# Optimization experiments

Measured on AMD Instinct MI355X. Metric: run time of the kernel, lower is better.

Reference implementation:

```python
import jax, jax.numpy as jnp
import numpy as np

C_CURV = 1.0      # curvature
EPS = 1e-4        # matches torch epsilon=0.0001
ATTN_SCALE = 0.12
NUM_HEADS = 16
HEAD_DIM = 64


def _sqnorm(x):
    return jnp.sum(x * x, axis=-1, keepdims=True)


def mobius_add(x, y, c):
    xn2, yn2 = _sqnorm(x), _sqnorm(y)
    ip = jnp.sum(x * y, axis=-1, keepdims=True)
    num = (1 + 2 * c * ip + c * yn2) * x + (1 - c * xn2) * y
    den = jnp.maximum(1 + 2 * c * ip + c * c * xn2 * yn2, EPS)
    return num / den


def logmap(x, u, c):
    sf = 2.0 / (1.0 + c * _sqnorm(x))                      # scaling factor at x
    mob = mobius_add(-x, u, c)
    mn = jnp.sqrt(_sqnorm(mob))
    cf = 2.0 / (sf * jnp.sqrt(c) + EPS)
    arg = jnp.clip(jnp.sqrt(c * mn), -0.99, 0.99)          # matches torch clamp on sqrt(c*norm)
    return cf * jnp.arctanh(arg) * mob / (mn + EPS)


def expmap(x, v, c):
    sf = 2.0 / (1.0 + c * _sqnorm(x))
    vn = jnp.sqrt(_sqnorm(v))
    arg = jnp.sqrt(jnp.clip(c * sf * vn * vn / 2.0, 0.0, 8.0))
    second = (1.0 / jnp.sqrt(c)) * jnp.tanh(arg) * v / (vn + EPS)
    return mobius_add(x, second, c)


def rms_norm(x):
    return x * jax.lax.rsqrt(jnp.mean(x * x, axis=-1, keepdims=True) + 1.1920929e-07)


def rotary_tables(T, head_dim):
    # dim//4 geometric freqs, padded with dim//4 zeros -> dim//2 total
    freqs = (1.0 / 1024.0) ** jnp.linspace(0.0, 1.0, head_dim // 4, dtype=jnp.float32)
    freqs = jnp.concatenate([freqs, jnp.zeros(head_dim // 4, dtype=jnp.float32)])
    theta = jnp.arange(T, dtype=jnp.float32)[:, None] * freqs[None, :]   # [T, hd/2]
    return jnp.cos(theta), jnp.sin(theta)


def apply_rotary(x, cos, sin):
    # x: [B,T,H,hd]; cos/sin: [T,hd/2]
    x1, x2 = jnp.split(x, 2, axis=-1)
    c = cos[None, :, None, :]
    s = sin[None, :, None, :]
    return jnp.concatenate([x1 * c + x2 * s, -x1 * s + x2 * c], axis=-1)


def setup_inputs() -> dict:
    key = jax.random.key(0)
    k1, k2, k3 = jax.random.split(key, 3)
    B, T, dim = 1, 2048, 1024
    hdim = NUM_HEADS * HEAD_DIM
    std = 0.5 * dim ** (-0.5)
    bound = (3.0 ** 0.5) * std
    x = jax.random.normal(k1, (B, T, dim), dtype=jnp.float32)
    qkv_w = jax.random.uniform(k2, (3, hdim, dim), dtype=jnp.float32, minval=-bound, maxval=bound)
    # original zero-inits c_proj; use small random weights for a non-degenerate baseline
    c_proj_w = jax.random.uniform(k3, (dim, hdim), dtype=jnp.float32, minval=-bound, maxval=bound)
    return {"x": x, "qkv_w": qkv_w, "c_proj_w": c_proj_w}


def reference(x, qkv_w, c_proj_w):
    B, T, dim = x.shape
    H, hd = NUM_HEADS, HEAD_DIM
    c = C_CURV

    # reference point: previous token (origin for first position)
    ref = jnp.pad(x[:, :-1, :], ((0, 0), (1, 0), (0, 0)))
    x_hyp = logmap(ref, x, c)

    # fused QKV projection: [B,T,3*hdim] -> q,k,v [B,T,H,hd]
    qkv = jnp.einsum('btd,ehd->bteh', x_hyp, qkv_w)            # e=3, h=hdim
    q, k, v = (qkv[:, :, i, :].reshape(B, T, H, hd) for i in range(3))

    cos, sin = rotary_tables(T, hd)
    q = apply_rotary(rms_norm(q), cos, sin)
    k = apply_rotary(rms_norm(k), cos, sin)

    # causal attention with fixed scale 0.12 (BlockMask here = standard causal)
    scores = jnp.einsum('bqhd,bkhd->bhqk', q, k) * ATTN_SCALE
    causal = jnp.tril(jnp.ones((T, T), dtype=bool))
    scores = jnp.where(causal[None, None], scores, -jnp.inf)
    p = jax.nn.softmax(scores, axis=-1)
    y = jnp.einsum('bhqk,bkhd->bqhd', p, v).reshape(B, T, H * hd)

    y = y @ c_proj_w.T
    y = expmap(ref, y, c)   # map_back_after_attention=True
    return y, ref
```

## Files before the change

kernel.cpp:

```cpp
#include <hip/hip_runtime.h>
#include <math.h>

#define T_SEQ 2048
#define DIM   1024
#define HD3   3072
#define NH    16
#define HD    64
#define EPSF  1e-4f
#define MB    1048576

typedef __attribute__((ext_vector_type(8))) short bf16x8;
typedef __attribute__((ext_vector_type(4))) float f32x4;
typedef __attribute__((ext_vector_type(16))) float f32x16;
typedef __attribute__((ext_vector_type(4))) unsigned int u32x4;

__device__ __forceinline__ ushort f2bf(float f) {
  unsigned int u = __float_as_uint(f);
  unsigned int r = (u + 0x7FFFu + ((u >> 16) & 1u)) >> 16;
  return (ushort)r;
}
__device__ __forceinline__ float bf2f(ushort u) {
  return __uint_as_float(((unsigned int)u) << 16);
}
__device__ __forceinline__ unsigned int pk2(float a, float b) {
  unsigned int r;
  asm("v_cvt_pk_bf16_f32 %0, %1, %2" : "=v"(r) : "v"(a), "v"(b));
  return r;
}

#define GLOAD(gp, lp) __builtin_amdgcn_global_load_lds( \
    (const __attribute__((address_space(1))) unsigned int*)(gp), \
    (__attribute__((address_space(3))) unsigned int*)(lp), 16, 0, 0)

__device__ __forceinline__ float blockSum(float v, float* s4) {
#pragma unroll
  for (int o = 32; o > 0; o >>= 1) v += __shfl_xor(v, o, 64);
  __syncthreads();
  if ((threadIdx.x & 63) == 0) s4[threadIdx.x >> 6] = v;
  __syncthreads();
  return s4[0] + s4[1] + s4[2] + s4[3];
}

__global__ void logmap_cvt(const float* __restrict__ x,
                           ushort* __restrict__ xhyp,
                           float* __restrict__ ref_out,
                           const float* __restrict__ wa,
                           const float* __restrict__ wb,
                           ushort* __restrict__ da,
                           ushort* __restrict__ db) {
  if (blockIdx.x >= T_SEQ) {
    int i = (blockIdx.x - T_SEQ) * 256 + threadIdx.x;
    const float* src; ushort* dst; int j;
    if (i < 393216) { src = wa; dst = da; j = i; }
    else            { src = wb; dst = db; j = i - 393216; }
    float4 a = ((const float4*)src)[j * 2];
    float4 b = ((const float4*)src)[j * 2 + 1];
    bf16x8 v;
    v[0] = f2bf(a.x); v[1] = f2bf(a.y); v[2] = f2bf(a.z); v[3] = f2bf(a.w);
    v[4] = f2bf(b.x); v[5] = f2bf(b.y); v[6] = f2bf(b.z); v[7] = f2bf(b.w);
    *(bf16x8*)(dst + (size_t)j * 8) = v;
    return;
  }
  __shared__ float s4[4];
  int t = blockIdx.x;
  const float* xt = x + (size_t)t * DIM;
  float xe[4], re[4];
  float xn2 = 0.f, yn2 = 0.f, ip = 0.f;
#pragma unroll
  for (int i = 0; i < 4; i++) {
    int e = threadIdx.x + i * 256;
    float xv = xt[e];
    float rv = (t > 0) ? xt[e - DIM] : 0.f;
    xe[i] = xv; re[i] = rv;
    yn2 += xv * xv;
    xn2 += rv * rv;
    ip  -= rv * xv;
    ref_out[(size_t)t * DIM + e] = rv;
  }
  xn2 = blockSum(xn2, s4);
  yn2 = blockSum(yn2, s4);
  ip  = blockSum(ip,  s4);
  float a = 1.f + 2.f * ip + yn2;
  float b = 1.f - xn2;
  float den = fmaxf(1.f + 2.f * ip + xn2 * yn2, EPSF);
  float invden = 1.f / den;
  float mob[4];
  float mn2 = 0.f;
#pragma unroll
  for (int i = 0; i < 4; i++) {
    float m = (-a * re[i] + b * xe[i]) * invden;
    mob[i] = m;
    mn2 += m * m;
  }
  mn2 = blockSum(mn2, s4);
  float mn  = sqrtf(mn2);
  float sf  = 2.f / (1.f + xn2);
  float cf  = 2.f / (sf + EPSF);
  float arg = fminf(sqrtf(mn), 0.99f);
  float mult = cf * atanhf(arg) / (mn + EPSF);
#pragma unroll
  for (int i = 0; i < 4; i++)
    xhyp[(size_t)t * DIM + threadIdx.x + i * 256] = f2bf(mult * mob[i]);
}

template<int BM>
__global__ __launch_bounds__(256) void gemm_bf16(const ushort* __restrict__ A,
                                                 const ushort* __restrict__ W,
                                                 float* __restrict__ C,
                                                 int M, int N, int K) {
  __shared__ ushort As[2][BM * 32];
  __shared__ ushort Bs[2][128 * 32];
  constexpr int NF = (BM == 128) ? 4 : 2;
  int tid = threadIdx.x;
  int lane = tid & 63, w = tid >> 6;
  int row_base = (BM == 128) ? (w >> 1) * 64 : 0;
  int col_base = (BM == 128) ? (w & 1) * 64 : w * 32;
  int g = lane >> 4, cc = lane & 15;
  int bm = blockIdx.y * BM, bn = blockIdx.x * 128;
  f32x4 acc[4][NF] = {};

  {
    if constexpr (BM == 128) {
#pragma unroll
      for (int i = 0; i < 2; i++) {
        int ch = i * 256 + tid;
        GLOAD(A + (size_t)(bm + (ch >> 2)) * K + (ch & 3) * 8, &As[0][ch * 8]);
      }
    } else {
      int ch = tid;
      GLOAD(A + (size_t)(bm + (ch >> 2)) * K + (ch & 3) * 8, &As[0][ch * 8]);
    }
#pragma unroll
    for (int i = 0; i < 2; i++) {
      int ch = i * 256 + tid;
      GLOAD(W + (size_t)(bn + (ch >> 2)) * K + (ch & 3) * 8, &Bs[0][ch * 8]);
    }
  }
  __syncthreads();

  int cur = 0;
  for (int kt = 0; kt < K; kt += 32) {
    if (kt + 32 < K) {
      int nxt = cur ^ 1;
      if constexpr (BM == 128) {
#pragma unroll
        for (int i = 0; i < 2; i++) {
          int ch = i * 256 + tid;
          GLOAD(A + (size_t)(bm + (ch >> 2)) * K + kt + 32 + (ch & 3) * 8, &As[nxt][ch * 8]);
        }
      } else {
        int ch = tid;
        GLOAD(A + (size_t)(bm + (ch >> 2)) * K + kt + 32 + (ch & 3) * 8, &As[nxt][ch * 8]);
      }
#pragma unroll
      for (int i = 0; i < 2; i++) {
        int ch = i * 256 + tid;
        GLOAD(W + (size_t)(bn + (ch >> 2)) * K + kt + 32 + (ch & 3) * 8, &Bs[nxt][ch * 8]);
      }
    }
    bf16x8 af[4], bfr[NF];
#pragma unroll
    for (int m = 0; m < 4; m++)
      af[m] = *(const bf16x8*)&As[cur][(row_base + m * 16 + cc) * 32 + 8 * g];
#pragma unroll
    for (int n = 0; n < NF; n++)
      bfr[n] = *(const bf16x8*)&Bs[cur][(col_base + n * 16 + cc) * 32 + 8 * g];
#pragma unroll
    for (int m = 0; m < 4; m++)
#pragma unroll
      for (int n = 0; n < NF; n++)
        acc[m][n] = __builtin_amdgcn_mfma_f32_16x16x32_bf16(af[m], bfr[n], acc[m][n], 0, 0, 0);
    __syncthreads();
    cur ^= 1;
  }
#pragma unroll
  for (int m = 0; m < 4; m++)
#pragma unroll
    for (int n = 0; n < NF; n++)
#pragma unroll
      for (int j = 0; j < 4; j++)
        C[(size_t)(bm + row_base + m * 16 + g * 4 + j) * N + bn + col_base + n * 16 + cc] = acc[m][n][j];
}

__global__ __launch_bounds__(256) void rmsrot_vtrans(const float* __restrict__ qkvf,
                                                     ushort* __restrict__ qfr,
                                                     ushort* __restrict__ kfr,
                                                     ushort* __restrict__ vfr) {
  __shared__ ushort qtile[64][64];
  __shared__ ushort ktile[64][64];
  __shared__ ushort vtile[64][64];
  int h = blockIdx.y, tt = blockIdx.x;
  int w = threadIdx.x >> 6, lane = threadIdx.x & 63;
  int j = lane & 31;
  float freq = 0.f;
  bool dotrig = (j < 16);
  if (dotrig) freq = exp2f(-(10.f / 15.f) * (float)j);
#pragma unroll 4
  for (int i = 0; i < 16; i++) {
    int r = w * 16 + i;
    int t = tt * 64 + r;
    const float* base = qkvf + (size_t)t * HD3;
    float qv = base[h * HD + lane];
    float kv = base[DIM + h * HD + lane];
    float qs = qv * qv, ks = kv * kv;
#pragma unroll
    for (int o = 32; o > 0; o >>= 1) {
      qs += __shfl_xor(qs, o, 64);
      ks += __shfl_xor(ks, o, 64);
    }
    float qn = qv * rsqrtf(qs * (1.f / 64.f) + 1.1920929e-07f);
    float kn = kv * rsqrtf(ks * (1.f / 64.f) + 1.1920929e-07f);
    float cth = 1.f, sth = 0.f;
    if (dotrig) {
      float th = (float)t * freq;
      cth = cosf(th);
      sth = sinf(th);
    }
    float qp = __shfl_xor(qn, 32, 64);
    float kp = __shfl_xor(kn, 32, 64);
    float sgn = (lane < 32) ? 1.f : -1.f;
    int pc = lane ^ ((r & 7) << 3);
    qtile[r][pc] = f2bf(qn * cth + sgn * qp * sth);
    ktile[r][pc] = f2bf(kn * cth + sgn * kp * sth);
  }
#pragma unroll
  for (int i = 0; i < 16; i++) {
    int r = w + i * 4;
    vtile[lane][r ^ ((lane & 7) << 3)] =
        f2bf(qkvf[(size_t)(tt * 64 + r) * HD3 + 2 * DIM + h * HD + lane]);
  }
  __syncthreads();
#pragma unroll
  for (int rd = 0; rd < 6; rd++) {
    int item = rd * 256 + threadIdx.x;
    int buf = item >> 9;
    int grp = (item >> 8) & 1;
    int st  = (item >> 6) & 3;
    int ln  = item & 63;
    int row = grp * 32 + (ln & 31);
    int col = st * 16 + 8 * (ln >> 5);
    int pc  = col ^ ((row & 7) << 3);
    bf16x8 v8;
    if (buf == 0)      v8 = *(const bf16x8*)&qtile[row][pc];
    else if (buf == 1) v8 = *(const bf16x8*)&ktile[row][pc];
    else               v8 = *(const bf16x8*)&vtile[row][pc];
    if (buf == 0) {
      size_t dst = (((size_t)h * 64 + tt * 2 + grp) * 4 + st) * 512 + ln * 8;
      *(bf16x8*)&qfr[dst] = v8;
    } else {
      size_t dst = ((((size_t)h * 32 + tt) * 2 + grp) * 4 + st) * 512 + ln * 8;
      if (buf == 1) *(bf16x8*)&kfr[dst] = v8;
      else          *(bf16x8*)&vfr[dst] = v8;
    }
  }
}

__global__ __launch_bounds__(256, 2) void attn_mfma(const ushort* __restrict__ qfr,
                                                    const ushort* __restrict__ kfr,
                                                    const ushort* __restrict__ vfr,
                                                    ushort* __restrict__ parts) {
  int lane = threadIdx.x & 63;
  int hi = lane >> 5;
  int q31 = lane & 31;
  int w = threadIdx.x >> 6;
  int tid = blockIdx.x * 4 + w;
  int h = tid / 288;
  int s = tid % 288;
  int g = (int)((sqrtf((float)s + 1.0f) - 1.0f) * 0.5f);
  while (4 * (g + 1) * (g + 2) <= s) ++g;
  while (4 * g * (g + 1) > s) --g;
  int rem = s - 4 * g * (g + 1);
  int qi8 = rem / (g + 1);
  int ch  = rem - qi8 * (g + 1);
  int qt  = 8 * g + qi8;
  int qbase  = qt * 32;
  int kstart = ch * 256;
  int kend   = min(kstart + 256, qbase + 32);
  bool fin   = (kend == qbase + 32);
  int nt     = (kend - kstart + 63) >> 6;

  bf16x8 qf[4];
  {
    const ushort* qb8 = qfr + (((size_t)h * 64 + qt) * 4) * 512 + lane * 8;
#pragma unroll
    for (int st = 0; st < 4; st++)
      qf[st] = *(const bf16x8*)(qb8 + st * 512);
  }

  f32x16 acc0 = {}, acc1 = {};
  float lrow = 0.f;
  int qglob = qbase + q31;
  const float SC = 0.12f * 1.44269504f;

  for (int ti = 0; ti < nt; ti++) {
    int k0 = kstart + ti * 64;
    int kblk = k0 >> 6;
    const ushort* kb8 = kfr + ((((size_t)h * 32 + kblk) * 2) * 4) * 512 + lane * 8;
    const ushort* vb8 = vfr + ((((size_t)h * 32 + kblk) * 2) * 4) * 512 + lane * 8;
    f32x16 cA = {}, cB = {};
#pragma unroll
    for (int st = 0; st < 4; st++) {
      bf16x8 kfa = *(const bf16x8*)(kb8 + st * 512);
      bf16x8 kfb = *(const bf16x8*)(kb8 + (4 + st) * 512);
      cA = __builtin_amdgcn_mfma_f32_32x32x16_bf16(kfa, qf[st], cA, 0, 0, 0);
      cB = __builtin_amdgcn_mfma_f32_32x32x16_bf16(kfb, qf[st], cB, 0, 0, 0);
    }
    float p[32];
#pragma unroll
    for (int r = 0; r < 16; r++) {
      float sA = cA[r] * SC;
      float sB = cB[r] * SC;
      if (fin) {
        int key = k0 + (r & 3) + 8 * (r >> 2) + 4 * hi;
        if (key > qglob)      sA = -1e30f;
        if (key + 32 > qglob) sB = -1e30f;
      }
      p[r] = sA;
      p[16 + r] = sB;
    }
    float rs0 = 0.f, rs1 = 0.f;
#pragma unroll
    for (int r = 0; r < 16; r++) {
      p[r]      = exp2f(p[r]);      rs0 += p[r];
      p[16 + r] = exp2f(p[16 + r]); rs1 += p[16 + r];
    }
    float rs = rs0 + rs1;
    rs += __shfl_xor(rs, 32, 64);
    lrow += rs;
    unsigned int pw[16], sw[16];
#pragma unroll
    for (int j = 0; j < 16; j++)
      pw[j] = pk2(p[2 * j], p[2 * j + 1]);
#pragma unroll
    for (int j = 0; j < 16; j++)
      sw[j] = __shfl_xor(pw[j], 32, 64);
    u32x4 u0, u1, u2, u3;
    u0[0] = hi ? sw[2]  : pw[0];
    u0[1] = hi ? sw[3]  : pw[1];
    u0[2] = hi ? pw[2]  : sw[0];
    u0[3] = hi ? pw[3]  : sw[1];
    u1[0] = hi ? sw[6]  : pw[4];
    u1[1] = hi ? sw[7]  : pw[5];
    u1[2] = hi ? pw[6]  : sw[4];
    u1[3] = hi ? pw[7]  : sw[5];
    u2[0] = hi ? sw[10] : pw[8];
    u2[1] = hi ? sw[11] : pw[9];
    u2[2] = hi ? pw[10] : sw[8];
    u2[3] = hi ? pw[11] : sw[9];
    u3[0] = hi ? sw[14] : pw[12];
    u3[1] = hi ? sw[15] : pw[13];
    u3[2] = hi ? pw[14] : sw[12];
    u3[3] = hi ? pw[15] : sw[13];
    bf16x8 pbA0 = __builtin_bit_cast(bf16x8, u0);
    bf16x8 pbA1 = __builtin_bit_cast(bf16x8, u1);
    bf16x8 pbB0 = __builtin_bit_cast(bf16x8, u2);
    bf16x8 pbB1 = __builtin_bit_cast(bf16x8, u3);
    {
      bf16x8 vA0 = *(const bf16x8*)(vb8 + 0 * 512);
      bf16x8 vA1 = *(const bf16x8*)(vb8 + 1 * 512);
      bf16x8 vA2 = *(const bf16x8*)(vb8 + 2 * 512);
      bf16x8 vA3 = *(const bf16x8*)(vb8 + 3 * 512);
      acc0 = __builtin_amdgcn_mfma_f32_32x32x16_bf16(vA0, pbA0, acc0, 0, 0, 0);
      acc0 = __builtin_amdgcn_mfma_f32_32x32x16_bf16(vA1, pbA1, acc0, 0, 0, 0);
      acc0 = __builtin_amdgcn_mfma_f32_32x32x16_bf16(vA2, pbB0, acc0, 0, 0, 0);
      acc0 = __builtin_amdgcn_mfma_f32_32x32x16_bf16(vA3, pbB1, acc0, 0, 0, 0);
      bf16x8 vB0 = *(const bf16x8*)(vb8 + 4 * 512);
      bf16x8 vB1 = *(const bf16x8*)(vb8 + 5 * 512);
      bf16x8 vB2 = *(const bf16x8*)(vb8 + 6 * 512);
      bf16x8 vB3 = *(const bf16x8*)(vb8 + 7 * 512);
      acc1 = __builtin_amdgcn_mfma_f32_32x32x16_bf16(vB0, pbA0, acc1, 0, 0, 0);
      acc1 = __builtin_amdgcn_mfma_f32_32x32x16_bf16(vB1, pbA1, acc1, 0, 0, 0);
      acc1 = __builtin_amdgcn_mfma_f32_32x32x16_bf16(vB2, pbB0, acc1, 0, 0, 0);
      acc1 = __builtin_amdgcn_mfma_f32_32x32x16_bf16(vB3, pbB1, acc1, 0, 0, 0);
    }
  }
  ushort* rec = parts + (size_t)(h * 288 + s) * 2176;
#pragma unroll
  for (int r = 0; r < 16; r++) {
    int d = (r & 3) + 8 * (r >> 2) + 4 * hi;
    rec[q31 * 64 + d]      = f2bf(acc0[r]);
    rec[q31 * 64 + 32 + d] = f2bf(acc1[r]);
  }
  if (!hi)
    *(float*)((char*)rec + 4096 + q31 * 4) = lrow;
}

__global__ __launch_bounds__(256) void attn_merge(const ushort* __restrict__ parts,
                                                  ushort* __restrict__ o) {
  int w = threadIdx.x >> 6, lane = threadIdx.x & 63;
  int idx = blockIdx.x * 4 + w;
  int r = idx & 31;
  int rec_i = idx >> 5;
  int qt = rec_i & 63, h = rec_i >> 6;
  int g = qt >> 3, rr = qt & 7;
  int nch = g + 1;
  int off = qt + 4 * g * (g - 1) + rr * g;
  const ushort* base = parts + (size_t)(h * 288 + off) * 2176;
  float L = 0.f, ov = 0.f;
#pragma unroll
  for (int i = 0; i < 8; i++) {
    if (i < nch) {
      L  += *(const float*)((const char*)base + i * 4352 + 4096 + r * 4);
      ov += bf2f(base[i * 2176 + r * 64 + lane]);
    }
  }
  o[(size_t)(qt * 32 + r) * DIM + h * HD + lane] = f2bf(ov / L);
}

__global__ void expmap_kernel(const float* __restrict__ y2,
                              const float* __restrict__ ref,
                              float* __restrict__ yout) {
  __shared__ float s4[4];
  int t = blockIdx.x;
  float xe[4], ve[4];
  float xn2 = 0.f, vn2 = 0.f, xv = 0.f;
#pragma unroll
  for (int i = 0; i < 4; i++) {
    int e = threadIdx.x + i * 256;
    float X = ref[(size_t)t * DIM + e];
    float V = y2[(size_t)t * DIM + e];
    xe[i] = X; ve[i] = V;
    xn2 += X * X; vn2 += V * V; xv += X * V;
  }
  xn2 = blockSum(xn2, s4);
  vn2 = blockSum(vn2, s4);
  xv  = blockSum(xv,  s4);
  float vn  = sqrtf(vn2);
  float sf  = 2.f / (1.f + xn2);
  float arg = sqrtf(fminf(fmaxf(0.5f * sf * vn2, 0.f), 8.f));
  float scl = tanhf(arg) / (vn + EPSF);
  float yn2 = scl * scl * vn2;
  float ip  = scl * xv;
  float A = 1.f + 2.f * ip + yn2;
  float B = (1.f - xn2) * scl;
  float den = fmaxf(1.f + 2.f * ip + xn2 * yn2, EPSF);
  float invden = 1.f / den;
#pragma unroll
  for (int i = 0; i < 4; i++)
    yout[(size_t)t * DIM + threadIdx.x + i * 256] = (A * xe[i] + B * ve[i]) * invden;
}

extern "C" void kernel_launch(void* const* d_in, const int* in_sizes, int n_in,
                              void* d_out, int out_size, void* d_ws, size_t ws_size,
                              hipStream_t stream) {
  const float* x        = (const float*)d_in[0];
  const float* qkv_w    = (const float*)d_in[1];
  const float* c_proj_w = (const float*)d_in[2];
  float* out = (float*)d_out;
  char*  W   = (char*)d_ws;

  ushort* qkvw_bf   = (ushort*)(W);
  ushort* cprojw_bf = (ushort*)(W + 6  * MB);
  ushort* xhyp_bf   = (ushort*)(W + 8  * MB);
  float*  qkvf      = (float*) (W + 12 * MB);
  ushort* qfrag     = (ushort*)(W + 36 * MB);
  ushort* kfrag     = (ushort*)(W + 40 * MB);
  ushort* vfrag     = (ushort*)(W + 44 * MB);
  ushort* parts     = (ushort*)(W + 12 * MB);
  ushort* obuf      = xhyp_bf;
  float*  y2        = qkvf;
  float*  ref       = out + (size_t)T_SEQ * DIM;

  logmap_cvt<<<T_SEQ + 2048, 256, 0, stream>>>(x, xhyp_bf, ref, qkv_w, c_proj_w,
                                               qkvw_bf, cprojw_bf);
  gemm_bf16<128><<<dim3(HD3 / 128, T_SEQ / 128), 256, 0, stream>>>(xhyp_bf, qkvw_bf, qkvf, T_SEQ, HD3, DIM);
  rmsrot_vtrans<<<dim3(T_SEQ / 64, NH), 256, 0, stream>>>(qkvf, qfrag, kfrag, vfrag);
  attn_mfma<<<1152, 256, 0, stream>>>(qfrag, kfrag, vfrag, parts);
  attn_merge<<<8192, 256, 0, stream>>>(parts, obuf);
  gemm_bf16<64><<<dim3(DIM / 128, T_SEQ / 64), 256, 0, stream>>>(obuf, cprojw_bf, y2, T_SEQ, DIM, DIM);
  expmap_kernel<<<T_SEQ, 256, 0, stream>>>(y2, ref, out);
}
```

Before: 121.0 us.

## Fuse RMS norm, rotary and fragment layout into QKV GEMM epilogue

Removes the separate rmsrot_vtrans kernel by doing RMS normalisation, rotary embedding, bf16 conversion and the swizzled fragment layout (including the V transpose) directly in the QKV GEMM epilogue. Each wave's 64x64 accumulator tile maps to one head, so the row norm is reduced with lane shuffles. This avoids writing and re-reading the 24 MB fp32 QKV intermediate and saves one launch. In exchange it adds 32 KB of shared memory per block, which may lower GEMM occupancy, and puts more epilogue work on the GEMM.

Measured after the change: 109.1 us. 1.11x faster.

```diff
diff --git a/kernel.cpp b/kernel.cpp
--- a/kernel.cpp
+++ b/kernel.cpp
@@ -103,13 +103,17 @@
     xhyp[(size_t)t * DIM + threadIdx.x + i * 256] = f2bf(mult * mob[i]);
 }
 
-template<int BM>
+template<int BM, int EPI>
 __global__ __launch_bounds__(256) void gemm_bf16(const ushort* __restrict__ A,
                                                  const ushort* __restrict__ W,
                                                  float* __restrict__ C,
+                                                 ushort* __restrict__ qfr,
+                                                 ushort* __restrict__ kfr,
+                                                 ushort* __restrict__ vfr,
                                                  int M, int N, int K) {
   __shared__ ushort As[2][BM * 32];
   __shared__ ushort Bs[2][128 * 32];
+  __shared__ ushort etile[EPI ? 4 * 64 * 64 : 4];
   constexpr int NF = (BM == 128) ? 4 : 2;
   int tid = threadIdx.x;
   int lane = tid & 63, w = tid >> 6;
@@ -173,85 +177,81 @@
     __syncthreads();
     cur ^= 1;
   }
-#pragma unroll
-  for (int m = 0; m < 4; m++)
-#pragma unroll
-    for (int n = 0; n < NF; n++)
-#pragma unroll
-      for (int j = 0; j < 4; j++)
-        C[(size_t)(bm + row_base + m * 16 + g * 4 + j) * N + bn + col_base + n * 16 + cc] = acc[m][n][j];
-}
-
-__global__ __launch_bounds__(256) void rmsrot_vtrans(const float* __restrict__ qkvf,
-                                                     ushort* __restrict__ qfr,
-                                                     ushort* __restrict__ kfr,
-                                                     ushort* __restrict__ vfr) {
-  __shared__ ushort qtile[64][64];
-  __shared__ ushort ktile[64][64];
-  __shared__ ushort vtile[64][64];
-  int h = blockIdx.y, tt = blockIdx.x;
-  int w = threadIdx.x >> 6, lane = threadIdx.x & 63;
-  int j = lane & 31;
-  float freq = 0.f;
-  bool dotrig = (j < 16);
-  if (dotrig) freq = exp2f(-(10.f / 15.f) * (float)j);
-#pragma unroll 4
-  for (int i = 0; i < 16; i++) {
-    int r = w * 16 + i;
-    int t = tt * 64 + r;
-    const float* base = qkvf + (size_t)t * HD3;
-    float qv = base[h * HD + lane];
-    float kv = base[DIM + h * HD + lane];
-    float qs = qv * qv, ks = kv * kv;
-#pragma unroll
-    for (int o = 32; o > 0; o >>= 1) {
-      qs += __shfl_xor(qs, o, 64);
-      ks += __shfl_xor(ks, o, 64);
-    }
-    float qn = qv * rsqrtf(qs * (1.f / 64.f) + 1.1920929e-07f);
-    float kn = kv * rsqrtf(ks * (1.f / 64.f) + 1.1920929e-07f);
-    float cth = 1.f, sth = 0.f;
-    if (dotrig) {
-      float th = (float)t * freq;
-      cth = cosf(th);
-      sth = sinf(th);
-    }
-    float qp = __shfl_xor(qn, 32, 64);
-    float kp = __shfl_xor(kn, 32, 64);
-    float sgn = (lane < 32) ? 1.f : -1.f;
-    int pc = lane ^ ((r & 7) << 3);
-    qtile[r][pc] = f2bf(qn * cth + sgn * qp * sth);
-    ktile[r][pc] = f2bf(kn * cth + sgn * kp * sth);
-  }
-#pragma unroll
-  for (int i = 0; i < 16; i++) {
-    int r = w + i * 4;
-    vtile[lane][r ^ ((lane & 7) << 3)] =
-        f2bf(qkvf[(size_t)(tt * 64 + r) * HD3 + 2 * DIM + h * HD + lane]);
-  }
-  __syncthreads();
-#pragma unroll
-  for (int rd = 0; rd < 6; rd++) {
-    int item = rd * 256 + threadIdx.x;
-    int buf = item >> 9;
-    int grp = (item >> 8) & 1;
-    int st  = (item >> 6) & 3;
-    int ln  = item & 63;
-    int row = grp * 32 + (ln & 31);
-    int col = st * 16 + 8 * (ln >> 5);
-    int pc  = col ^ ((row & 7) << 3);
-    bf16x8 v8;
-    if (buf == 0)      v8 = *(const bf16x8*)&qtile[row][pc];
-    else if (buf == 1) v8 = *(const bf16x8*)&ktile[row][pc];
-    else               v8 = *(const bf16x8*)&vtile[row][pc];
-    if (buf == 0) {
-      size_t dst = (((size_t)h * 64 + tt * 2 + grp) * 4 + st) * 512 + ln * 8;
-      *(bf16x8*)&qfr[dst] = v8;
+
+  if constexpr (EPI == 0) {
+#pragma unroll
+    for (int m = 0; m < 4; m++)
+#pragma unroll
+      for (int n = 0; n < NF; n++)
+#pragma unroll
+        for (int j = 0; j < 4; j++)
+          C[(size_t)(bm + row_base + m * 16 + g * 4 + j) * N + bn + col_base + n * 16 + cc] = acc[m][n][j];
+  } else {
+    ushort (*tile)[64] = (ushort(*)[64])&etile[w * 4096];
+    int bx = blockIdx.x;
+    int region = bx >> 3;
+    int hh = ((bx & 7) << 1) | (w & 1);
+    int tokbase = blockIdx.y * 128 + (w >> 1) * 64;
+    if (region < 2) {
+      float rinv[4][4];
+#pragma unroll
+      for (int m = 0; m < 4; m++)
+#pragma unroll
+        for (int j = 0; j < 4; j++) {
+          float ss = acc[m][0][j] * acc[m][0][j] + acc[m][1][j] * acc[m][1][j]
+                   + acc[m][2][j] * acc[m][2][j] + acc[m][3][j] * acc[m][3][j];
+          ss += __shfl_xor(ss, 1, 64);
+          ss += __shfl_xor(ss, 2, 64);
+          ss += __shfl_xor(ss, 4, 64);
+          ss += __shfl_xor(ss, 8, 64);
+          rinv[m][j] = rsqrtf(ss * (1.f / 64.f) + 1.1920929e-07f);
+        }
+      float freq = exp2f(-(10.f / 15.f) * (float)cc);
+#pragma unroll
+      for (int m = 0; m < 4; m++)
+#pragma unroll
+        for (int j = 0; j < 4; j++) {
+          int row = m * 16 + g * 4 + j;
+          float sth, cth;
+          sincosf((float)(tokbase + row) * freq, &sth, &cth);
+          float ri = rinv[m][j];
+          float x0 = acc[m][0][j] * ri;
+          float x2 = acc[m][2][j] * ri;
+          int sz = (row & 7) << 3;
+          tile[row][(0 * 16 + cc) ^ sz] = f2bf(x0 * cth + x2 * sth);
+          tile[row][(1 * 16 + cc) ^ sz] = f2bf(acc[m][1][j] * ri);
+          tile[row][(2 * 16 + cc) ^ sz] = f2bf(-x0 * sth + x2 * cth);
+          tile[row][(3 * 16 + cc) ^ sz] = f2bf(acc[m][3][j] * ri);
+        }
     } else {
-      size_t dst = ((((size_t)h * 32 + tt) * 2 + grp) * 4 + st) * 512 + ln * 8;
-      if (buf == 1) *(bf16x8*)&kfr[dst] = v8;
-      else          *(bf16x8*)&vfr[dst] = v8;
-    }
+#pragma unroll
+      for (int m = 0; m < 4; m++)
+#pragma unroll
+        for (int n = 0; n < 4; n++)
+#pragma unroll
+          for (int j = 0; j < 4; j++) {
+            int trow = m * 16 + g * 4 + j;
+            int d = n * 16 + cc;
+            tile[d][trow ^ ((d & 7) << 3)] = f2bf(acc[m][n][j]);
+          }
+    }
+    int q31 = lane & 31, hi = lane >> 5;
+#pragma unroll
+    for (int grp = 0; grp < 2; grp++)
+#pragma unroll
+      for (int st = 0; st < 4; st++) {
+        int r = grp * 32 + q31;
+        bf16x8 v8 = *(const bf16x8*)&tile[r][(st * 16 + 8 * hi) ^ ((r & 7) << 3)];
+        if (region == 0) {
+          int qt = blockIdx.y * 4 + (w >> 1) * 2 + grp;
+          *(bf16x8*)&qfr[(((size_t)hh * 64 + qt) * 4 + st) * 512 + lane * 8] = v8;
+        } else {
+          int kblk = blockIdx.y * 2 + (w >> 1);
+          size_t dst = ((((size_t)hh * 32 + kblk) * 2 + grp) * 4 + st) * 512 + lane * 8;
+          if (region == 1) *(bf16x8*)&kfr[dst] = v8;
+          else             *(bf16x8*)&vfr[dst] = v8;
+        }
+      }
   }
 }
 
@@ -452,21 +452,21 @@
   ushort* qkvw_bf   = (ushort*)(W);
   ushort* cprojw_bf = (ushort*)(W + 6  * MB);
   ushort* xhyp_bf   = (ushort*)(W + 8  * MB);
-  float*  qkvf      = (float*) (W + 12 * MB);
+  float*  y2        = (float*) (W + 12 * MB);
+  ushort* parts     = (ushort*)(W + 12 * MB);
   ushort* qfrag     = (ushort*)(W + 36 * MB);
   ushort* kfrag     = (ushort*)(W + 40 * MB);
   ushort* vfrag     = (ushort*)(W + 44 * MB);
-  ushort* parts     = (ushort*)(W + 12 * MB);
   ushort* obuf      = xhyp_bf;
-  float*  y2        = qkvf;
   float*  ref       = out + (size_t)T_SEQ * DIM;
 
   logmap_cvt<<<T_SEQ + 2048, 256, 0, stream>>>(x, xhyp_bf, ref, qkv_w, c_proj_w,
                                                qkvw_bf, cprojw_bf);
-  gemm_bf16<128><<<dim3(HD3 / 128, T_SEQ / 128), 256, 0, stream>>>(xhyp_bf, qkvw_bf, qkvf, T_SEQ, HD3, DIM);
-  rmsrot_vtrans<<<dim3(T_SEQ / 64, NH), 256, 0, stream>>>(qkvf, qfrag, kfrag, vfrag);
+  gemm_bf16<128, 1><<<dim3(HD3 / 128, T_SEQ / 128), 256, 0, stream>>>(
+      xhyp_bf, qkvw_bf, nullptr, qfrag, kfrag, vfrag, T_SEQ, HD3, DIM);
   attn_mfma<<<1152, 256, 0, stream>>>(qfrag, kfrag, vfrag, parts);
   attn_merge<<<8192, 256, 0, stream>>>(parts, obuf);
-  gemm_bf16<64><<<dim3(DIM / 128, T_SEQ / 64), 256, 0, stream>>>(obuf, cprojw_bf, y2, T_SEQ, DIM, DIM);
+  gemm_bf16<64, 0><<<dim3(DIM / 128, T_SEQ / 64), 256, 0, stream>>>(
+      obuf, cprojw_bf, y2, nullptr, nullptr, nullptr, T_SEQ, DIM, DIM);
   expmap_kernel<<<T_SEQ, 256, 0, stream>>>(y2, ref, out);
 }
```
